# Optimization experiments

Hardware: AMD Instinct MI355X
Metric: run time of the kernel (lower is better)

Reference implementation:

```python
import jax, jax.numpy as jnp
import numpy as np

B, D = 1024, 512


def setup_inputs() -> dict:
    key = jax.random.key(0)
    k1, k2, k3 = jax.random.split(key, 3)
    x = jax.random.normal(k1, (B, D), dtype=jnp.float32)
    x_dot = jax.random.normal(k2, (B, D), dtype=jnp.float32)
    # linear score network weight: s(x) = x @ W^T  (scaled for sane magnitudes)
    W = jax.random.normal(k3, (D, D), dtype=jnp.float32) / np.sqrt(D).astype(np.float32)
    return {"x": x, "x_dot": x_dot, "W": W}


def reference(x, x_dot, W):
    # s(x): [b, d]
    s = x @ W.T
    d = x.shape[1]
    # g(x) = I + s s^T : [b, d, d]  (faithful to the original bmm formulation)
    G = jnp.eye(d, dtype=x.dtype)[None, :, :] + s[:, :, None] * s[:, None, :]
    # kinetic energy: x_dot^T G x_dot : [b]
    return jnp.einsum('bi,bij,bj->b', x_dot, G, x_dot)
```

## Files before the change

### kernel.cpp

```cpp
#include <hip/hip_runtime.h>

#define BB 1024
#define DD 512
#define BTILE 32
#define JTILE 128
#define ICH 64

__global__ __launch_bounds__(256, 4) void stm_main_kernel(
    const float* __restrict__ x, const float* __restrict__ xdot,
    const float* __restrict__ W, float* __restrict__ ws_t) {
  __shared__ float xd_t[ICH][BTILE];
  __shared__ float w_s[ICH][JTILE];

  const int tid = threadIdx.x;
  const int b0 = blockIdx.x * BTILE;
  const int j0 = blockIdx.y * JTILE;
  const int i0 = blockIdx.z * ICH;
  const int tb = tid >> 5;
  const int tj = tid & 31;

  {
    const int row = tid & 31;
    const int f4 = tid >> 5;
    const float4* src = (const float4*)(xdot + (size_t)(b0 + row) * DD + i0);
#pragma unroll
    for (int p = 0; p < 2; ++p) {
      const int c4 = f4 + p * 8;
      float4 v = src[c4];
      const int c = c4 * 4;
      xd_t[c + 0][row] = v.x; xd_t[c + 1][row] = v.y;
      xd_t[c + 2][row] = v.z; xd_t[c + 3][row] = v.w;
    }
  }
  {
#pragma unroll
    for (int v = 0; v < 8; ++v) {
      const int f4 = tid + v * 256;
      const int ii = f4 >> 5, jj4 = f4 & 31;
      *((float4*)&w_s[ii][jj4 * 4]) =
          ((const float4*)(W + (size_t)(i0 + ii) * DD + j0))[jj4];
    }
  }
  __syncthreads();

  float acc[4][4] = {};
#pragma unroll
  for (int i = 0; i < ICH; ++i) {
    const float4 xd = *(const float4*)&xd_t[i][tb * 4];
    const float4 w  = *(const float4*)&w_s[i][tj * 4];
    acc[0][0] += xd.x * w.x; acc[0][1] += xd.x * w.y;
    acc[0][2] += xd.x * w.z; acc[0][3] += xd.x * w.w;
    acc[1][0] += xd.y * w.x; acc[1][1] += xd.y * w.y;
    acc[1][2] += xd.y * w.z; acc[1][3] += xd.y * w.w;
    acc[2][0] += xd.z * w.x; acc[2][1] += xd.z * w.y;
    acc[2][2] += xd.z * w.z; acc[2][3] += xd.z * w.w;
    acc[3][0] += xd.w * w.x; acc[3][1] += xd.w * w.y;
    acc[3][2] += xd.w * w.z; acc[3][3] += xd.w * w.w;
  }

  float tp[4];
#pragma unroll
  for (int r = 0; r < 4; ++r) {
    const float4 xv =
        ((const float4*)(x + (size_t)(b0 + tb * 4 + r) * DD + j0))[tj];
    tp[r] = acc[r][0] * xv.x + acc[r][1] * xv.y +
            acc[r][2] * xv.z + acc[r][3] * xv.w;
  }
#pragma unroll
  for (int off = 16; off >= 1; off >>= 1) {
#pragma unroll
    for (int r = 0; r < 4; ++r) tp[r] += __shfl_xor(tp[r], off);
  }
  if (tj == 0) {
#pragma unroll
    for (int r = 0; r < 4; ++r)
      atomicAdd(ws_t + b0 + tb * 4 + r, tp[r]);
  }
}

__global__ __launch_bounds__(256) void stm_final_kernel(
    const float* __restrict__ xdot, const float* __restrict__ ws_t,
    float* __restrict__ out) {
  const int tid = threadIdx.x;
  const int wv = tid >> 6, ln = tid & 63;
  const int b = blockIdx.x * 4 + wv;
  const float4* xd4 = (const float4*)(xdot + (size_t)b * DD);
  float4 a = xd4[ln];
  float4 c = xd4[64 + ln];
  float n = a.x * a.x + a.y * a.y + a.z * a.z + a.w * a.w +
            c.x * c.x + c.y * c.y + c.z * c.z + c.w * c.w;
#pragma unroll
  for (int off = 32; off >= 1; off >>= 1) n += __shfl_xor(n, off);
  if (ln == 0) {
    const float t = ws_t[b];
    out[b] = n + t * t;
  }
}

extern "C" void kernel_launch(void* const* d_in, const int* in_sizes, int n_in,
                              void* d_out, int out_size, void* d_ws, size_t ws_size,
                              hipStream_t stream) {
  const float* x    = (const float*)d_in[0];
  const float* xdot = (const float*)d_in[1];
  const float* W    = (const float*)d_in[2];
  float* ws = (float*)d_ws;
  float* out = (float*)d_out;

  hipMemsetAsync(ws, 0, BB * sizeof(float), stream);

  dim3 g1(BB / BTILE, DD / JTILE, DD / ICH);
  stm_main_kernel<<<g1, 256, 0, stream>>>(x, xdot, W, ws);
  stm_final_kernel<<<BB / 4, 256, 0, stream>>>(xdot, ws, out);
}
```

Before: 73.33 us.

## Use 128x128 tiles with 8x8 register blocking and deterministic partial-sum workspace

The main kernel now uses 128-row by 128-column tiles with a 16-wide reduction chunk, and each thread computes an 8x8 register block instead of 4x4, which raises arithmetic intensity per shared-memory load. Atomic accumulation into one workspace vector is replaced by writing per-block partial sums into a [128][BB] workspace. The final kernel reduces those partials, so the memset launch is no longer needed. The trade-offs are a larger workspace read in the final kernel, higher register pressure under the launch bound of 4 blocks per CU, and a smaller K chunk per block.

After: 237.2 us. 3.23x slower.

```diff
diff --git a/kernel.cpp b/kernel.cpp
--- a/kernel.cpp
+++ b/kernel.cpp
@@ -2,79 +2,84 @@
 
 #define BB 1024
 #define DD 512
-#define BTILE 32
-#define JTILE 128
-#define ICH 64
+#define RT 128
+#define CT 128
+#define KT 16
+#define NIC (DD / KT)
+#define NP ((DD / CT) * NIC)
 
 __global__ __launch_bounds__(256, 4) void stm_main_kernel(
     const float* __restrict__ x, const float* __restrict__ xdot,
     const float* __restrict__ W, float* __restrict__ ws_t) {
-  __shared__ float xd_t[ICH][BTILE];
-  __shared__ float w_s[ICH][JTILE];
+  __shared__ float xd_s[RT][KT];
+  __shared__ float w_s[KT][CT];
 
   const int tid = threadIdx.x;
-  const int b0 = blockIdx.x * BTILE;
-  const int j0 = blockIdx.y * JTILE;
-  const int i0 = blockIdx.z * ICH;
-  const int tb = tid >> 5;
-  const int tj = tid & 31;
+  const int b0 = blockIdx.x * RT;
+  const int j0 = blockIdx.y * CT;
+  const int i0 = blockIdx.z * KT;
+  const int tb = tid >> 4;
+  const int tj = tid & 15;
 
-  {
-    const int row = tid & 31;
-    const int f4 = tid >> 5;
-    const float4* src = (const float4*)(xdot + (size_t)(b0 + row) * DD + i0);
 #pragma unroll
-    for (int p = 0; p < 2; ++p) {
-      const int c4 = f4 + p * 8;
-      float4 v = src[c4];
-      const int c = c4 * 4;
-      xd_t[c + 0][row] = v.x; xd_t[c + 1][row] = v.y;
-      xd_t[c + 2][row] = v.z; xd_t[c + 3][row] = v.w;
-    }
+  for (int v = 0; v < 2; ++v) {
+    const int idx = tid + v * 256;
+    const int row = idx >> 2, c4 = idx & 3;
+    *(float4*)&xd_s[row][c4 * 4] =
+        *(const float4*)(xdot + (size_t)(b0 + row) * DD + i0 + c4 * 4);
   }
-  {
 #pragma unroll
-    for (int v = 0; v < 8; ++v) {
-      const int f4 = tid + v * 256;
-      const int ii = f4 >> 5, jj4 = f4 & 31;
-      *((float4*)&w_s[ii][jj4 * 4]) =
-          ((const float4*)(W + (size_t)(i0 + ii) * DD + j0))[jj4];
-    }
+  for (int v = 0; v < 2; ++v) {
+    const int idx = tid + v * 256;
+    const int ii = idx >> 5, jj4 = idx & 31;
+    *(float4*)&w_s[ii][jj4 * 4] =
+        *(const float4*)(W + (size_t)(i0 + ii) * DD + j0 + jj4 * 4);
   }
   __syncthreads();
 
-  float acc[4][4] = {};
+  float acc[8][8] = {};
 #pragma unroll
-  for (int i = 0; i < ICH; ++i) {
-    const float4 xd = *(const float4*)&xd_t[i][tb * 4];
-    const float4 w  = *(const float4*)&w_s[i][tj * 4];
-    acc[0][0] += xd.x * w.x; acc[0][1] += xd.x * w.y;
-    acc[0][2] += xd.x * w.z; acc[0][3] += xd.x * w.w;
-    acc[1][0] += xd.y * w.x; acc[1][1] += xd.y * w.y;
-    acc[1][2] += xd.y * w.z; acc[1][3] += xd.y * w.w;
-    acc[2][0] += xd.z * w.x; acc[2][1] += xd.z * w.y;
-    acc[2][2] += xd.z * w.z; acc[2][3] += xd.z * w.w;
-    acc[3][0] += xd.w * w.x; acc[3][1] += xd.w * w.y;
-    acc[3][2] += xd.w * w.z; acc[3][3] += xd.w * w.w;
+  for (int i2 = 0; i2 < KT; i2 += 2) {
+    float2 xd[8];
+#pragma unroll
+    for (int r = 0; r < 8; ++r)
+      xd[r] = *(const float2*)&xd_s[tb * 8 + r][i2];
+#pragma unroll
+    for (int s = 0; s < 2; ++s) {
+      const float4 wlo = *(const float4*)&w_s[i2 + s][tj * 8];
+      const float4 whi = *(const float4*)&w_s[i2 + s][tj * 8 + 4];
+#pragma unroll
+      for (int r = 0; r < 8; ++r) {
+        const float a = s ? xd[r].y : xd[r].x;
+        acc[r][0] += a * wlo.x; acc[r][1] += a * wlo.y;
+        acc[r][2] += a * wlo.z; acc[r][3] += a * wlo.w;
+        acc[r][4] += a * whi.x; acc[r][5] += a * whi.y;
+        acc[r][6] += a * whi.z; acc[r][7] += a * whi.w;
+      }
+    }
   }
 
-  float tp[4];
+  float tp[8];
 #pragma unroll
-  for (int r = 0; r < 4; ++r) {
-    const float4 xv =
-        ((const float4*)(x + (size_t)(b0 + tb * 4 + r) * DD + j0))[tj];
-    tp[r] = acc[r][0] * xv.x + acc[r][1] * xv.y +
-            acc[r][2] * xv.z + acc[r][3] * xv.w;
+  for (int r = 0; r < 8; ++r) {
+    const float* xr = x + (size_t)(b0 + tb * 8 + r) * DD + j0 + tj * 8;
+    const float4 xlo = *(const float4*)xr;
+    const float4 xhi = *(const float4*)(xr + 4);
+    tp[r] = acc[r][0] * xlo.x + acc[r][1] * xlo.y +
+            acc[r][2] * xlo.z + acc[r][3] * xlo.w +
+            acc[r][4] * xhi.x + acc[r][5] * xhi.y +
+            acc[r][6] * xhi.z + acc[r][7] * xhi.w;
   }
 #pragma unroll
-  for (int off = 16; off >= 1; off >>= 1) {
+  for (int off = 8; off >= 1; off >>= 1) {
 #pragma unroll
-    for (int r = 0; r < 4; ++r) tp[r] += __shfl_xor(tp[r], off);
+    for (int r = 0; r < 8; ++r) tp[r] += __shfl_xor(tp[r], off);
   }
   if (tj == 0) {
-#pragma unroll
-    for (int r = 0; r < 4; ++r)
-      atomicAdd(ws_t + b0 + tb * 4 + r, tp[r]);
+    const int p = blockIdx.y * NIC + blockIdx.z;
+    float* dst = ws_t + (size_t)p * BB + b0 + tb * 8;
+    *(float4*)(dst + 0) = make_float4(tp[0], tp[1], tp[2], tp[3]);
+    *(float4*)(dst + 4) = make_float4(tp[4], tp[5], tp[6], tp[7]);
   }
 }
 
@@ -85,16 +90,17 @@
   const int wv = tid >> 6, ln = tid & 63;
   const int b = blockIdx.x * 4 + wv;
   const float4* xd4 = (const float4*)(xdot + (size_t)b * DD);
-  float4 a = xd4[ln];
-  float4 c = xd4[64 + ln];
+  const float4 a = xd4[ln];
+  const float4 c = xd4[64 + ln];
   float n = a.x * a.x + a.y * a.y + a.z * a.z + a.w * a.w +
             c.x * c.x + c.y * c.y + c.z * c.z + c.w * c.w;
+  float t = ws_t[(size_t)ln * BB + b] + ws_t[(size_t)(ln + 64) * BB + b];
 #pragma unroll
-  for (int off = 32; off >= 1; off >>= 1) n += __shfl_xor(n, off);
-  if (ln == 0) {
-    const float t = ws_t[b];
-    out[b] = n + t * t;
+  for (int off = 32; off >= 1; off >>= 1) {
+    n += __shfl_xor(n, off);
+    t += __shfl_xor(t, off);
   }
+  if (ln == 0) out[b] = n + t * t;
 }
 
 extern "C" void kernel_launch(void* const* d_in, const int* in_sizes, int n_in,
@@ -106,9 +112,7 @@
   float* ws = (float*)d_ws;
   float* out = (float*)d_out;
 
-  hipMemsetAsync(ws, 0, BB * sizeof(float), stream);
-
-  dim3 g1(BB / BTILE, DD / JTILE, DD / ICH);
+  dim3 g1(BB / RT, DD / CT, NIC);
   stm_main_kernel<<<g1, 256, 0, stream>>>(x, xdot, W, ws);
   stm_final_kernel<<<BB / 4, 256, 0, stream>>>(xdot, ws, out);
 }
```
